# Kernel optimization log

Measured on AMD Instinct MI355X. Metric: run time of the kernel, lower is better.

Reference implementation:

```python
import jax, jax.numpy as jnp
import numpy as np

N_H, N_O, D = 5000, 15000, 1024
E_HH, E_OO, E_HO = 20000, 40000, 40000


def setup_inputs() -> dict:
    key = jax.random.key(0)
    ks = jax.random.split(key, 20)
    N = N_H + N_O
    w = lambda k, shp: jax.random.normal(k, shp, dtype=jnp.float32) * 0.02
    inp = {
        'n_f': jax.random.normal(ks[0], (N, D), dtype=jnp.float32),
        'src_hh': jax.random.randint(ks[1], (E_HH,), 0, N_H),
        'dst_hh': jax.random.randint(ks[2], (E_HH,), 0, N_H),
        'src_oo': jax.random.randint(ks[3], (E_OO,), 0, N_O) + N_H,
        'dst_oo': jax.random.randint(ks[4], (E_OO,), 0, N_O) + N_H,
        'src_ho': jax.random.randint(ks[5], (E_HO,), 0, N_H),
        'dst_ho': jax.random.randint(ks[6], (E_HO,), 0, N_O) + N_H,
        'W_hh': w(ks[7], (2 * D, D)), 'b_hh': jnp.zeros((D,), jnp.float32),
        'W_oo': w(ks[8], (2 * D, D)), 'b_oo': jnp.zeros((D,), jnp.float32),
        'W_ho': w(ks[9], (2 * D, D)), 'b_ho': jnp.zeros((D,), jnp.float32),
        'W_att': w(ks[10], (D, 1)), 'b_att': jnp.zeros((1,), jnp.float32),
        'W_hn': w(ks[11], (2 * D, D)), 'b_hn': jnp.zeros((D,), jnp.float32),
        'W_on': w(ks[12], (2 * D, D)), 'b_on': jnp.zeros((D,), jnp.float32),
    }
    return inp


def reference(n_f, src_hh, dst_hh, src_oo, dst_oo, src_ho, dst_ho,
              W_hh, b_hh, W_oo, b_oo, W_ho, b_ho, W_att, b_att,
              W_hn, b_hn, W_on, b_on):
    N = n_f.shape[0]

    def edge_mlp(src, dst, W, b):
        # gather -> concat -> Linear -> ReLU  (H_H/O_O/H_O EdgeApplyModule)
        feat = jnp.concatenate([n_f[src], n_f[dst]], axis=1)  # [E, 2D]
        return jax.nn.relu(feat @ W + b)                       # [E, D]

    e_f = jnp.concatenate([
        edge_mlp(src_hh, dst_hh, W_hh, b_hh),
        edge_mlp(src_oo, dst_oo, W_oo, b_oo),
        edge_mlp(src_ho, dst_ho, W_ho, b_ho),
    ], axis=0)                                                 # [E, D]
    src = jnp.concatenate([src_hh, src_oo, src_ho])
    dst = jnp.concatenate([dst_hh, dst_oo, dst_ho])

    # E_AttentionModule: per-edge scalar attention logit
    a = (e_f @ W_att + b_att)[:, 0]                            # [E]

    # update_all: per-destination softmax over incoming edges (mailbox softmax)
    seg_max = jax.ops.segment_max(a, dst, num_segments=N)
    seg_max = jnp.where(jnp.isfinite(seg_max), seg_max, 0.0)
    ex = jnp.exp(a - seg_max[dst])
    denom = jax.ops.segment_sum(ex, dst, num_segments=N)
    alpha = ex / jnp.where(denom[dst] == 0, 1.0, denom[dst])   # [E]
    z = jax.ops.segment_sum(alpha[:, None] * n_f[src], dst, num_segments=N)  # [N, D]

    # Node apply: concat(n_f, z_f) -> Linear -> ReLU, separate h/o MLPs
    new_h = jax.nn.relu(jnp.concatenate([n_f[:N_H], z[:N_H]], axis=1) @ W_hn + b_hn)
    new_o = jax.nn.relu(jnp.concatenate([n_f[N_H:], z[N_H:]], axis=1) @ W_on + b_on)
    return jnp.concatenate([new_h, new_o], axis=0)             # [N, D] new_n_f
```

## Files before the change

kernel.cpp:

```cpp
#include <hip/hip_runtime.h>

#define N_H   5000
#define N_O   15000
#define N_TOT 20000
#define DD    1024
#define E_HH  20000
#define E_OO  40000
#define E_HO  40000
#define E_TOT 100000

typedef unsigned short u16;
typedef unsigned int u32;
typedef __attribute__((ext_vector_type(8))) short short8;
typedef __attribute__((ext_vector_type(4))) float f32x4;
typedef const __attribute__((address_space(1))) u32 gas_u32;
typedef __attribute__((address_space(3))) u32 las_u32;

__device__ __forceinline__ float bf2f(u16 u) {
    union { unsigned int i; float f; } v; v.i = ((unsigned int)u) << 16; return v.f;
}
__device__ __forceinline__ u16 f2bf(float f) {
    union { float f; unsigned int i; } v; v.f = f;
    unsigned int u = v.i;
    return (u16)((u + 0x7FFFu + ((u >> 16) & 1u)) >> 16);
}

__global__ void cast_bf(const float* __restrict__ in, u16* __restrict__ out) {
    size_t i = ((size_t)blockIdx.x * 256 + threadIdx.x) * 8;
    float4 a = *(const float4*)(in + i);
    float4 b = *(const float4*)(in + i + 4);
    u16 o[8] = {f2bf(a.x), f2bf(a.y), f2bf(a.z), f2bf(a.w),
                f2bf(b.x), f2bf(b.y), f2bf(b.z), f2bf(b.w)};
    *(uint4*)(out + i) = *(const uint4*)o;
}

struct TW  { const float* W; u16* dT; u16* dB; int ld; };
struct TW5 { TW t[5]; };
__global__ void transpose_all(TW5 p) {
    __shared__ float tile[32][33];
    int z = blockIdx.z;
    TW tw = p.t[z >> 1];
    int half = z & 1;
    int bk = blockIdx.x, bn = blockIdx.y;
    int tx = threadIdx.x & 31, ty = threadIdx.x >> 5;
#pragma unroll
    for (int yy = 0; yy < 4; yy++) {
        int k = half * 1024 + bk * 32 + ty + yy * 8;
        int n = bn * 32 + tx;
        tile[ty + yy * 8][tx] = tw.W[(size_t)k * 1024 + n];
    }
    __syncthreads();
    u16* dst = half ? tw.dB : tw.dT;
#pragma unroll
    for (int yy = 0; yy < 4; yy++) {
        int n = bn * 32 + ty + yy * 8;
        int k = bk * 32 + tx;
        dst[(size_t)n * tw.ld + k] = f2bf(tile[tx][ty + yy * 8]);
    }
}

#define PROJ_NBM_H 40
#define PROJ_NBM_O 118
#define PROJ_NBN   24
__launch_bounds__(256)
__global__ void gemm_proj(const u16* __restrict__ Ah, const u16* __restrict__ Ao,
                          const u16* __restrict__ Bth, const u16* __restrict__ Bto,
                          u16* __restrict__ Ch, u16* __restrict__ Co) {
    __shared__ u16 smem[2][128][64];
    int bid = (blockIdx.x & 7) * ((PROJ_NBM_H + PROJ_NBM_O) * PROJ_NBN / 8)
            + (blockIdx.x >> 3);
    const u16* A; const u16* Bt; u16* C; int M;
    if (bid < PROJ_NBM_H * PROJ_NBN) { A = Ah; Bt = Bth; C = Ch; M = N_H; }
    else { bid -= PROJ_NBM_H * PROJ_NBN; A = Ao; Bt = Bto; C = Co; M = N_O; }
    int bm = bid / PROJ_NBN, bn = bid % PROJ_NBN;
    int t = threadIdx.x;
    int wave = t >> 6, lane = t & 63;
    int wr = wave >> 1, wc = wave & 1;
    int lm = lane & 15, q = lane >> 4;
    f32x4 acc[4][4] = {};
    int srow = lane >> 3;
    int scol = ((lane & 7) ^ srow) * 8;

    for (int k0 = 0; k0 < 1024; k0 += 64) {
#pragma unroll
        for (int it = 0; it < 4; it++) {
            int chunk = wave * 4 + it;
            int row = chunk * 8 + srow;
            int gr = bm * 128 + row; if (gr >= M) gr = M - 1;
            __builtin_amdgcn_global_load_lds((gas_u32*)(A + (size_t)gr * 1024 + k0 + scol),
                                             (las_u32*)&smem[0][chunk * 8][0], 16, 0, 0);
            __builtin_amdgcn_global_load_lds((gas_u32*)(Bt + (size_t)(bn * 128 + row) * 1024 + k0 + scol),
                                             (las_u32*)&smem[1][chunk * 8][0], 16, 0, 0);
        }
        __syncthreads();
#pragma unroll
        for (int ks = 0; ks < 64; ks += 32) {
            short8 af[4], bfr[4];
            int pc = (((ks >> 3) + q) ^ (lm & 7)) * 8;
#pragma unroll
            for (int i = 0; i < 4; i++)
                af[i] = *(const short8*)&smem[0][wr * 64 + i * 16 + lm][pc];
#pragma unroll
            for (int j = 0; j < 4; j++)
                bfr[j] = *(const short8*)&smem[1][wc * 64 + j * 16 + lm][pc];
#pragma unroll
            for (int i = 0; i < 4; i++)
#pragma unroll
                for (int j = 0; j < 4; j++)
                    acc[i][j] = __builtin_amdgcn_mfma_f32_16x16x32_bf16(af[i], bfr[j], acc[i][j], 0, 0, 0);
        }
        __syncthreads();
    }
    u16* sc = &smem[0][0][0];
#pragma unroll
    for (int i = 0; i < 4; i++)
#pragma unroll
        for (int j = 0; j < 4; j++)
#pragma unroll
            for (int r = 0; r < 4; r++)
                sc[(wr * 64 + i * 16 + q * 4 + r) * 128 + (wc * 64 + j * 16 + lm)] =
                    f2bf(acc[i][j][r]);
    __syncthreads();
#pragma unroll
    for (int it = 0; it < 8; it++) {
        int flat = it * 256 + t;
        int r = flat >> 4, cs = (flat & 15) * 8;
        int grow = bm * 128 + r;
        if (grow < M)
            *(uint4*)&C[(size_t)grow * 3072 + bn * 128 + cs] = *(const uint4*)&sc[r * 128 + cs];
    }
}

#define NODE_NBM_H 40
#define NODE_NBM_O 118
#define NODE_NBN   8
__launch_bounds__(256)
__global__ void gemm_node(const u16* __restrict__ nf_h, const u16* __restrict__ nf_o,
                          const u16* __restrict__ z_h, const u16* __restrict__ z_o,
                          const u16* __restrict__ Bthn, const u16* __restrict__ Bton,
                          const float* __restrict__ b_hn, const float* __restrict__ b_on,
                          float* __restrict__ out_h, float* __restrict__ out_o) {
    __shared__ u16 lA[128][64];
    __shared__ u16 lB[128][64];
    int bid = (blockIdx.x & 7) * ((NODE_NBM_H + NODE_NBM_O) * NODE_NBN / 8)
            + (blockIdx.x >> 3);
    const u16 *A0, *A1, *Bt; const float* bias; float* C; int M;
    if (bid < NODE_NBM_H * NODE_NBN) {
        A0 = nf_h; A1 = z_h; Bt = Bthn; bias = b_hn; C = out_h; M = N_H;
    } else {
        bid -= NODE_NBM_H * NODE_NBN;
        A0 = nf_o; A1 = z_o; Bt = Bton; bias = b_on; C = out_o; M = N_O;
    }
    int bm = bid / NODE_NBN, bn = bid % NODE_NBN;
    int t = threadIdx.x;
    int wave = t >> 6, lane = t & 63;
    int wr = wave >> 1, wc = wave & 1;
    int lm = lane & 15, q = lane >> 4;
    f32x4 acc[4][4] = {};
    int srow = lane >> 3;
    int scol = ((lane & 7) ^ srow) * 8;

    for (int k0 = 0; k0 < 2048; k0 += 64) {
        const u16* Asrc = (k0 < 1024) ? A0 : A1;
        int kk = k0 & 1023;
#pragma unroll
        for (int it = 0; it < 4; it++) {
            int chunk = wave * 4 + it;
            int row = chunk * 8 + srow;
            int gr = bm * 128 + row; if (gr >= M) gr = M - 1;
            __builtin_amdgcn_global_load_lds((gas_u32*)(Asrc + (size_t)gr * 1024 + kk + scol),
                                             (las_u32*)&lA[chunk * 8][0], 16, 0, 0);
            __builtin_amdgcn_global_load_lds((gas_u32*)(Bt + (size_t)(bn * 128 + row) * 2048 + k0 + scol),
                                             (las_u32*)&lB[chunk * 8][0], 16, 0, 0);
        }
        __syncthreads();
#pragma unroll
        for (int ks = 0; ks < 64; ks += 32) {
            short8 af[4], bfr[4];
            int pc = (((ks >> 3) + q) ^ (lm & 7)) * 8;
#pragma unroll
            for (int i = 0; i < 4; i++)
                af[i] = *(const short8*)&lA[wr * 64 + i * 16 + lm][pc];
#pragma unroll
            for (int j = 0; j < 4; j++)
                bfr[j] = *(const short8*)&lB[wc * 64 + j * 16 + lm][pc];
#pragma unroll
            for (int i = 0; i < 4; i++)
#pragma unroll
                for (int j = 0; j < 4; j++)
                    acc[i][j] = __builtin_amdgcn_mfma_f32_16x16x32_bf16(af[i], bfr[j], acc[i][j], 0, 0, 0);
        }
        __syncthreads();
    }
#pragma unroll
    for (int j = 0; j < 4; j++) {
        int col = bn * 128 + wc * 64 + j * 16 + lm;
        float bv = bias[col];
#pragma unroll
        for (int i = 0; i < 4; i++) {
            int row0 = bm * 128 + wr * 64 + i * 16 + q * 4;
#pragma unroll
            for (int r = 0; r < 4; r++) {
                int row = row0 + r;
                if (row < M)
                    C[(size_t)row * 1024 + col] = fmaxf(acc[i][j][r] + bv, 0.0f);
            }
        }
    }
}

__global__ void cat_edges(const int* __restrict__ shh, const int* __restrict__ dhh,
                          const int* __restrict__ soo, const int* __restrict__ doo,
                          const int* __restrict__ sho, const int* __restrict__ dho,
                          int* __restrict__ src_all, int* __restrict__ dst_all,
                          int* __restrict__ deg) {
    int e = blockIdx.x * 256 + threadIdx.x;
    if (e >= E_TOT) return;
    int s, d;
    if (e < E_HH)              { s = shh[e];               d = dhh[e]; }
    else if (e < E_HH + E_OO)  { s = soo[e - E_HH];        d = doo[e - E_HH]; }
    else                       { s = sho[e - E_HH - E_OO]; d = dho[e - E_HH - E_OO]; }
    src_all[e] = s; dst_all[e] = d;
    atomicAdd(&deg[d], 1);
}

__global__ void edge_att(const u16* __restrict__ proj_h, const u16* __restrict__ proj_o,
                         const float* __restrict__ b_hh, const float* __restrict__ b_oo,
                         const float* __restrict__ b_ho,
                         const float* __restrict__ W_att, const float* __restrict__ b_att,
                         const int* __restrict__ src_all, const int* __restrict__ dst_all,
                         float* __restrict__ a_out) {
    int wave = threadIdx.x >> 6, lane = threadIdx.x & 63;
    int e0 = blockIdx.x * 32 + wave * 8;
    const float* bsel = (e0 < E_HH) ? b_hh : (e0 < E_HH + E_OO ? b_oo : b_ho);
    float ww[16], bb[16];
#pragma unroll
    for (int i = 0; i < 16; i++) { ww[i] = W_att[lane * 16 + i]; bb[i] = bsel[lane * 16 + i]; }
    float batt = b_att[0];
#pragma unroll
    for (int k = 0; k < 8; k++) {
        int e = e0 + k;
        int s = src_all[e], d = dst_all[e];
        const u16 *u, *v;
        if (e < E_HH) {
            u = proj_h + (size_t)s * 3072;
            v = proj_h + (size_t)d * 3072 + 1024;
        } else if (e < E_HH + E_OO) {
            u = proj_o + (size_t)(s - N_H) * 3072;
            v = proj_o + (size_t)(d - N_H) * 3072 + 1024;
        } else {
            u = proj_h + (size_t)s * 3072 + 2048;
            v = proj_o + (size_t)(d - N_H) * 3072 + 2048;
        }
        int off = lane * 16;
        uint4 u0 = *(const uint4*)(u + off), u1 = *(const uint4*)(u + off + 8);
        uint4 v0 = *(const uint4*)(v + off), v1 = *(const uint4*)(v + off + 8);
        const u16* pu0 = (const u16*)&u0; const u16* pu1 = (const u16*)&u1;
        const u16* pv0 = (const u16*)&v0; const u16* pv1 = (const u16*)&v1;
        float acc = 0.f;
#pragma unroll
        for (int i = 0; i < 8; i++) {
            float tv = bf2f(pu0[i]) + bf2f(pv0[i]) + bb[i];
            acc += fmaxf(tv, 0.f) * ww[i];
        }
#pragma unroll
        for (int i = 0; i < 8; i++) {
            float tv = bf2f(pu1[i]) + bf2f(pv1[i]) + bb[8 + i];
            acc += fmaxf(tv, 0.f) * ww[8 + i];
        }
#pragma unroll
        for (int o = 32; o > 0; o >>= 1) acc += __shfl_down(acc, o);
        if (lane == 0) a_out[e] = acc + batt;
    }
}

__global__ void scan_deg(const int* __restrict__ deg, int* __restrict__ indptr) {
    __shared__ int sums[1024];
    int t = threadIdx.x;
    const int CH = 20;
    int beg = t * CH, end = beg + CH;
    if (end > N_TOT) end = N_TOT;
    if (beg > N_TOT) beg = N_TOT;
    int s = 0;
    for (int i = beg; i < end; i++) s += deg[i];
    sums[t] = s;
    __syncthreads();
    for (int off = 1; off < 1024; off <<= 1) {
        int v = sums[t];
        int add = (t >= off) ? sums[t - off] : 0;
        __syncthreads();
        sums[t] = v + add;
        __syncthreads();
    }
    int run = (t == 0) ? 0 : sums[t - 1];
    for (int i = beg; i < end; i++) { indptr[i] = run; run += deg[i]; }
    if (t == 1023) indptr[N_TOT] = sums[1023];
}

__global__ void fill_csr(const int* __restrict__ dst_all, const int* __restrict__ indptr,
                         int* __restrict__ cursor, int* __restrict__ edge_ids) {
    int e = blockIdx.x * 256 + threadIdx.x;
    if (e < E_TOT) {
        int d = dst_all[e];
        int pos = atomicAdd(&cursor[d], 1);
        edge_ids[indptr[d] + pos] = e;
    }
}

#define MAXDEG 1024
__global__ void soft_z(const float* __restrict__ a, const int* __restrict__ indptr,
                       const int* __restrict__ edge_ids, const int* __restrict__ src_all,
                       const u16* __restrict__ nf, u16* __restrict__ z) {
    __shared__ float s_a[MAXDEG];
    __shared__ int   s_src[MAXDEG];
    __shared__ float s_inv;
    int node = blockIdx.x;
    int t = threadIdx.x;
    int beg = indptr[node], end = indptr[node + 1];
    int deg = end - beg; if (deg > MAXDEG) deg = MAXDEG;
    if (t < 64) {
        float m = -1e30f;
        for (int i = t; i < deg; i += 64) {
            int eid = edge_ids[beg + i];
            float av = a[eid];
            s_a[i] = av;
            s_src[i] = src_all[eid];
            if (av > m) m = av;
        }
        for (int o = 32; o > 0; o >>= 1) m = fmaxf(m, __shfl_down(m, o));
        m = __shfl(m, 0);
        float ssum = 0.f;
        for (int i = t; i < deg; i += 64) {
            float ex = __expf(s_a[i] - m);
            s_a[i] = ex;
            ssum += ex;
        }
        for (int o = 32; o > 0; o >>= 1) ssum += __shfl_down(ssum, o);
        if (t == 0) s_inv = (ssum > 0.f) ? 1.0f / ssum : 0.f;
    }
    __syncthreads();
    float a0 = 0.f, a1 = 0.f, a2 = 0.f, a3 = 0.f;
    int base = t * 4;
    float inv = s_inv;
    for (int i = 0; i < deg; i++) {
        float al = s_a[i] * inv;
        const u16* row = nf + (size_t)s_src[i] * DD + base;
        uint2 p = *(const uint2*)row;
        const u16* pp = (const u16*)&p;
        a0 += al * bf2f(pp[0]); a1 += al * bf2f(pp[1]);
        a2 += al * bf2f(pp[2]); a3 += al * bf2f(pp[3]);
    }
    uint2 ov;
    u16* po = (u16*)&ov;
    po[0] = f2bf(a0); po[1] = f2bf(a1); po[2] = f2bf(a2); po[3] = f2bf(a3);
    *(uint2*)(z + (size_t)node * DD + base) = ov;
}

extern "C" void kernel_launch(void* const* d_in, const int* in_sizes, int n_in,
                              void* d_out, int out_size, void* d_ws, size_t ws_size,
                              hipStream_t stream) {
    const float* nf   = (const float*)d_in[0];
    const int* shh    = (const int*)d_in[1];
    const int* dhh    = (const int*)d_in[2];
    const int* soo    = (const int*)d_in[3];
    const int* doo    = (const int*)d_in[4];
    const int* sho    = (const int*)d_in[5];
    const int* dho    = (const int*)d_in[6];
    const float* W_hh = (const float*)d_in[7];
    const float* b_hh = (const float*)d_in[8];
    const float* W_oo = (const float*)d_in[9];
    const float* b_oo = (const float*)d_in[10];
    const float* W_ho = (const float*)d_in[11];
    const float* b_ho = (const float*)d_in[12];
    const float* W_att= (const float*)d_in[13];
    const float* b_att= (const float*)d_in[14];
    const float* W_hn = (const float*)d_in[15];
    const float* b_hn = (const float*)d_in[16];
    const float* W_on = (const float*)d_in[17];
    const float* b_on = (const float*)d_in[18];
    float* out = (float*)d_out;

    char* ws = (char*)d_ws;
    size_t off = 0;
    auto alloc = [&](size_t bytes) -> char* {
        char* p = ws + off;
        off += (bytes + 255) & ~(size_t)255;
        return p;
    };
    u16* nf_bf = (u16*)alloc((size_t)N_TOT * DD * 2);
    u16* Bt_h  = (u16*)alloc((size_t)3072 * 1024 * 2);
    u16* Bt_o  = (u16*)alloc((size_t)3072 * 1024 * 2);
    u16* Bt_hn = (u16*)alloc((size_t)1024 * 2048 * 2);
    u16* Bt_on = (u16*)alloc((size_t)1024 * 2048 * 2);
    u16* proj_h = (u16*)alloc((size_t)N_H * 3072 * 2);
    u16* proj_o = (u16*)alloc((size_t)N_O * 3072 * 2);
    u16* z_bf   = proj_h;
    float* a_log  = (float*)alloc(E_TOT * 4);
    int* src_all  = (int*)alloc(E_TOT * 4);
    int* dst_all  = (int*)alloc(E_TOT * 4);
    int* deg      = (int*)alloc(2 * N_TOT * 4);
    int* cursor   = deg + N_TOT;
    int* indptr   = (int*)alloc((N_TOT + 1) * 4);
    int* edge_ids = (int*)alloc(E_TOT * 4);
    (void)ws_size; (void)in_sizes; (void)n_in; (void)out_size;

    cast_bf<<<(N_TOT * DD) / (256 * 8), 256, 0, stream>>>(nf, nf_bf);
    TW5 tws;
    tws.t[0] = {W_hh, Bt_h,                       Bt_h + (size_t)1024 * 1024, 1024};
    tws.t[1] = {W_oo, Bt_o,                       Bt_o + (size_t)1024 * 1024, 1024};
    tws.t[2] = {W_ho, Bt_h + (size_t)2048 * 1024, Bt_o + (size_t)2048 * 1024, 1024};
    tws.t[3] = {W_hn, Bt_hn,                      Bt_hn + 1024,               2048};
    tws.t[4] = {W_on, Bt_on,                      Bt_on + 1024,               2048};
    transpose_all<<<dim3(32, 32, 10), 256, 0, stream>>>(tws);

    hipMemsetAsync(deg, 0, 2 * N_TOT * 4, stream);
    cat_edges<<<(E_TOT + 255) / 256, 256, 0, stream>>>(shh, dhh, soo, doo, sho, dho,
                                                       src_all, dst_all, deg);

    const u16* nf_bf_o = nf_bf + (size_t)N_H * DD;
    gemm_proj<<<(PROJ_NBM_H + PROJ_NBM_O) * PROJ_NBN, 256, 0, stream>>>(
        nf_bf, nf_bf_o, Bt_h, Bt_o, proj_h, proj_o);

    edge_att<<<E_TOT / 32, 256, 0, stream>>>(proj_h, proj_o, b_hh, b_oo, b_ho,
                                             W_att, b_att, src_all, dst_all, a_log);

    scan_deg<<<1, 1024, 0, stream>>>(deg, indptr);
    fill_csr<<<(E_TOT + 255) / 256, 256, 0, stream>>>(dst_all, indptr, cursor, edge_ids);

    soft_z<<<N_TOT, 256, 0, stream>>>(a_log, indptr, edge_ids, src_all, nf_bf, z_bf);

    gemm_node<<<(NODE_NBM_H + NODE_NBM_O) * NODE_NBN, 256, 0, stream>>>(
        nf_bf, nf_bf_o, z_bf, z_bf + (size_t)N_H * DD, Bt_hn, Bt_on,
        b_hn, b_on, out, out + (size_t)N_H * DD);
}
```

Measured before the change: 617.7 us.

## Fuse cast with edge concat, drop proj block swizzle, split node GEMM loop

The fp32→bf16 cast of node features and the edge-index concatenation/degree count are merged into one launch, removing a kernel launch. The XCD-style block-index swizzle in the projection GEMM is removed in favour of linear block order. The node GEMM K loop is split into two halves with per-half pointers, removing the per-iteration source select. The swizzle removal may change L2 locality across chiplets, which could hurt the projection GEMM.

```diff
diff --git a/kernel.cpp b/kernel.cpp
--- a/kernel.cpp
+++ b/kernel.cpp
@@ -25,13 +25,31 @@
     return (u16)((u + 0x7FFFu + ((u >> 16) & 1u)) >> 16);
 }
 
-__global__ void cast_bf(const float* __restrict__ in, u16* __restrict__ out) {
-    size_t i = ((size_t)blockIdx.x * 256 + threadIdx.x) * 8;
-    float4 a = *(const float4*)(in + i);
-    float4 b = *(const float4*)(in + i + 4);
-    u16 o[8] = {f2bf(a.x), f2bf(a.y), f2bf(a.z), f2bf(a.w),
-                f2bf(b.x), f2bf(b.y), f2bf(b.z), f2bf(b.w)};
-    *(uint4*)(out + i) = *(const uint4*)o;
+#define CAST_NB 10000
+__global__ void cast_cat(const float* __restrict__ in, u16* __restrict__ out,
+                         const int* __restrict__ shh, const int* __restrict__ dhh,
+                         const int* __restrict__ soo, const int* __restrict__ doo,
+                         const int* __restrict__ sho, const int* __restrict__ dho,
+                         int* __restrict__ src_all, int* __restrict__ dst_all,
+                         int* __restrict__ deg) {
+    int b = blockIdx.x;
+    if (b < CAST_NB) {
+        size_t i = ((size_t)b * 256 + threadIdx.x) * 8;
+        float4 a = *(const float4*)(in + i);
+        float4 c = *(const float4*)(in + i + 4);
+        u16 o[8] = {f2bf(a.x), f2bf(a.y), f2bf(a.z), f2bf(a.w),
+                    f2bf(c.x), f2bf(c.y), f2bf(c.z), f2bf(c.w)};
+        *(uint4*)(out + i) = *(const uint4*)o;
+        return;
+    }
+    int e = (b - CAST_NB) * 256 + threadIdx.x;
+    if (e >= E_TOT) return;
+    int s, d;
+    if (e < E_HH)              { s = shh[e];               d = dhh[e]; }
+    else if (e < E_HH + E_OO)  { s = soo[e - E_HH];        d = doo[e - E_HH]; }
+    else                       { s = sho[e - E_HH - E_OO]; d = dho[e - E_HH - E_OO]; }
+    src_all[e] = s; dst_all[e] = d;
+    atomicAdd(&deg[d], 1);
 }
 
 struct TW  { const float* W; u16* dT; u16* dB; int ld; };
@@ -67,8 +85,7 @@
                           const u16* __restrict__ Bth, const u16* __restrict__ Bto,
                           u16* __restrict__ Ch, u16* __restrict__ Co) {
     __shared__ u16 smem[2][128][64];
-    int bid = (blockIdx.x & 7) * ((PROJ_NBM_H + PROJ_NBM_O) * PROJ_NBN / 8)
-            + (blockIdx.x >> 3);
+    int bid = blockIdx.x;
     const u16* A; const u16* Bt; u16* C; int M;
     if (bid < PROJ_NBM_H * PROJ_NBN) { A = Ah; Bt = Bth; C = Ch; M = N_H; }
     else { bid -= PROJ_NBM_H * PROJ_NBN; A = Ao; Bt = Bto; C = Co; M = N_O; }
@@ -160,37 +177,39 @@
     int srow = lane >> 3;
     int scol = ((lane & 7) ^ srow) * 8;
 
-    for (int k0 = 0; k0 < 2048; k0 += 64) {
-        const u16* Asrc = (k0 < 1024) ? A0 : A1;
-        int kk = k0 & 1023;
-#pragma unroll
-        for (int it = 0; it < 4; it++) {
-            int chunk = wave * 4 + it;
-            int row = chunk * 8 + srow;
-            int gr = bm * 128 + row; if (gr >= M) gr = M - 1;
-            __builtin_amdgcn_global_load_lds((gas_u32*)(Asrc + (size_t)gr * 1024 + kk + scol),
-                                             (las_u32*)&lA[chunk * 8][0], 16, 0, 0);
-            __builtin_amdgcn_global_load_lds((gas_u32*)(Bt + (size_t)(bn * 128 + row) * 2048 + k0 + scol),
-                                             (las_u32*)&lB[chunk * 8][0], 16, 0, 0);
-        }
-        __syncthreads();
-#pragma unroll
-        for (int ks = 0; ks < 64; ks += 32) {
-            short8 af[4], bfr[4];
-            int pc = (((ks >> 3) + q) ^ (lm & 7)) * 8;
-#pragma unroll
-            for (int i = 0; i < 4; i++)
-                af[i] = *(const short8*)&lA[wr * 64 + i * 16 + lm][pc];
-#pragma unroll
-            for (int j = 0; j < 4; j++)
-                bfr[j] = *(const short8*)&lB[wc * 64 + j * 16 + lm][pc];
-#pragma unroll
-            for (int i = 0; i < 4; i++)
+    for (int half = 0; half < 2; half++) {
+        const u16* Asrc = half ? A1 : A0;
+        const u16* Bth = Bt + half * 1024;
+        for (int k0 = 0; k0 < 1024; k0 += 64) {
+#pragma unroll
+            for (int it = 0; it < 4; it++) {
+                int chunk = wave * 4 + it;
+                int row = chunk * 8 + srow;
+                int gr = bm * 128 + row; if (gr >= M) gr = M - 1;
+                __builtin_amdgcn_global_load_lds((gas_u32*)(Asrc + (size_t)gr * 1024 + k0 + scol),
+                                                 (las_u32*)&lA[chunk * 8][0], 16, 0, 0);
+                __builtin_amdgcn_global_load_lds((gas_u32*)(Bth + (size_t)(bn * 128 + row) * 2048 + k0 + scol),
+                                                 (las_u32*)&lB[chunk * 8][0], 16, 0, 0);
+            }
+            __syncthreads();
+#pragma unroll
+            for (int ks = 0; ks < 64; ks += 32) {
+                short8 af[4], bfr[4];
+                int pc = (((ks >> 3) + q) ^ (lm & 7)) * 8;
+#pragma unroll
+                for (int i = 0; i < 4; i++)
+                    af[i] = *(const short8*)&lA[wr * 64 + i * 16 + lm][pc];
 #pragma unroll
                 for (int j = 0; j < 4; j++)
-                    acc[i][j] = __builtin_amdgcn_mfma_f32_16x16x32_bf16(af[i], bfr[j], acc[i][j], 0, 0, 0);
-        }
-        __syncthreads();
+                    bfr[j] = *(const short8*)&lB[wc * 64 + j * 16 + lm][pc];
+#pragma unroll
+                for (int i = 0; i < 4; i++)
+#pragma unroll
+                    for (int j = 0; j < 4; j++)
+                        acc[i][j] = __builtin_amdgcn_mfma_f32_16x16x32_bf16(af[i], bfr[j], acc[i][j], 0, 0, 0);
+            }
+            __syncthreads();
+        }
     }
 #pragma unroll
     for (int j = 0; j < 4; j++) {
@@ -207,21 +226,6 @@
             }
         }
     }
-}
-
-__global__ void cat_edges(const int* __restrict__ shh, const int* __restrict__ dhh,
-                          const int* __restrict__ soo, const int* __restrict__ doo,
-                          const int* __restrict__ sho, const int* __restrict__ dho,
-                          int* __restrict__ src_all, int* __restrict__ dst_all,
-                          int* __restrict__ deg) {
-    int e = blockIdx.x * 256 + threadIdx.x;
-    if (e >= E_TOT) return;
-    int s, d;
-    if (e < E_HH)              { s = shh[e];               d = dhh[e]; }
-    else if (e < E_HH + E_OO)  { s = soo[e - E_HH];        d = doo[e - E_HH]; }
-    else                       { s = sho[e - E_HH - E_OO]; d = dho[e - E_HH - E_OO]; }
-    src_all[e] = s; dst_all[e] = d;
-    atomicAdd(&deg[d], 1);
 }
 
 __global__ void edge_att(const u16* __restrict__ proj_h, const u16* __restrict__ proj_o,
@@ -404,7 +408,10 @@
     int* edge_ids = (int*)alloc(E_TOT * 4);
     (void)ws_size; (void)in_sizes; (void)n_in; (void)out_size;
 
-    cast_bf<<<(N_TOT * DD) / (256 * 8), 256, 0, stream>>>(nf, nf_bf);
+    hipMemsetAsync(deg, 0, 2 * N_TOT * 4, stream);
+    cast_cat<<<CAST_NB + (E_TOT + 255) / 256, 256, 0, stream>>>(
+        nf, nf_bf, shh, dhh, soo, doo, sho, dho, src_all, dst_all, deg);
+
     TW5 tws;
     tws.t[0] = {W_hh, Bt_h,                       Bt_h + (size_t)1024 * 1024, 1024};
     tws.t[1] = {W_oo, Bt_o,                       Bt_o + (size_t)1024 * 1024, 1024};
@@ -413,10 +420,6 @@
     tws.t[4] = {W_on, Bt_on,                      Bt_on + 1024,               2048};
     transpose_all<<<dim3(32, 32, 10), 256, 0, stream>>>(tws);
 
-    hipMemsetAsync(deg, 0, 2 * N_TOT * 4, stream);
-    cat_edges<<<(E_TOT + 255) / 256, 256, 0, stream>>>(shh, dhh, soo, doo, sho, dho,
-                                                       src_all, dst_all, deg);
-
     const u16* nf_bf_o = nf_bf + (size_t)N_H * DD;
     gemm_proj<<<(PROJ_NBM_H + PROJ_NBM_O) * PROJ_NBN, 256, 0, stream>>>(
         nf_bf, nf_bf_o, Bt_h, Bt_o, proj_h, proj_o);
```

Result: no change. 609.9 us (-1.3%).
